# Kernel optimization log

Hardware: AMD Instinct MI355X
Metric: run time of the kernel (lower is better)

Reference implementation:

```python
import jax, jax.numpy as jnp
import numpy as np

TOP_K = 2          # routed top_k = top_k - num_shared_experts = 3 - 1
CAP_FACTOR = 1.1   # capacity_factor


def setup_inputs() -> dict:
    key = jax.random.key(0)
    ks = jax.random.split(key, 12)
    B, S, D, E = 4, 2048, 1024, 7
    s = 0.02
    return {
        "x": jax.random.normal(ks[0], (B, S, D), jnp.float32),
        "noise": jax.random.normal(ks[1], (B, S, E), jnp.float32),
        "Wr": jax.random.normal(ks[2], (D, E)) * s, "br": jnp.zeros((E,)),
        "Wn": jax.random.normal(ks[3], (D, E)) * s, "bn": jnp.zeros((E,)),
        "W1": jax.random.normal(ks[4], (E, D, D)) * s, "b1": jnp.zeros((E, D)),
        "W2": jax.random.normal(ks[5], (E, D, D)) * s, "b2": jnp.zeros((E, D)),
        "Ws1": jax.random.normal(ks[6], (D, D)) * s, "bs1": jnp.zeros((D,)),
        "Ws2": jax.random.normal(ks[7], (D, D)) * s, "bs2": jnp.zeros((D,)),
    }


def reference(x, noise, Wr, br, Wn, bn, W1, b1, W2, b2, Ws1, bs1, Ws2, bs2):
    B, S, D = x.shape
    E = Wr.shape[1]
    N = B * S
    C = int(N * TOP_K / E * CAP_FACTOR)  # per-expert capacity (static)

    # shared expert (Dropout inactive at inference)
    x_shared = jax.nn.relu(x @ Ws1 + bs1) @ Ws2 + bs2

    # --- noisy top-k router ---
    logits = x @ Wr + br
    noisy = logits + noise * jax.nn.softplus(x @ Wn + bn)
    vals, idx = jax.lax.top_k(noisy, TOP_K)                    # [B,S,K]
    onehot = jax.nn.one_hot(idx, E, dtype=x.dtype)             # [B,S,K,E]
    probs_k = jax.nn.softmax(vals, axis=-1)                    # softmax over -inf-masked logits == softmax over top-k vals
    router_probs = jnp.einsum('bske,bsk->bse', onehot, probs_k)
    expert_mask = onehot.sum(-2)
    lbl = E * (router_probs.mean((0, 1)) * expert_mask.mean((0, 1))).sum()

    # --- capacity-limited dispatch, first-come-first-served in flat token order ---
    flat_x = x.reshape(N, D)
    flat_g = router_probs.reshape(N, E)
    m = (expert_mask.reshape(N, E) > 0).T                      # [E,N] token->expert assignment
    pos = jnp.cumsum(m.astype(jnp.int32), axis=1) - 1          # slot within expert
    valid = m & (pos < C)
    token = jnp.arange(N, dtype=jnp.int32)
    dest = jnp.where(valid, jnp.arange(E, dtype=jnp.int32)[:, None] * C + pos, E * C)
    idxs = jnp.full((E * C + 1,), N, dtype=jnp.int32)
    idxs = idxs.at[dest.reshape(-1)].set(jnp.broadcast_to(token, (E, N)).reshape(-1))
    idxs = idxs[:E * C].reshape(E, C)                          # token id per slot, N = padding

    xpad = jnp.concatenate([flat_x, jnp.zeros((1, D), x.dtype)], axis=0)
    gpad = jnp.concatenate([flat_g, jnp.zeros((1, E), x.dtype)], axis=0)
    xe = xpad[idxs]                                            # [E,C,D]
    h = jax.nn.relu(jnp.einsum('ecd,edh->ech', xe, W1) + b1[:, None, :])
    out = jnp.einsum('ech,ehd->ecd', h, W2) + b2[:, None, :]
    g = (gpad[idxs] * jnp.eye(E, dtype=x.dtype)[:, None, :]).sum(-1)  # [E,C] gate per slot
    slot_valid = (idxs < N).astype(x.dtype)
    weighted = out * (g * slot_valid)[..., None]

    upd = jnp.zeros((N + 1, D), x.dtype).at[idxs.reshape(-1)].add(weighted.reshape(-1, D))[:N]
    final = upd.reshape(B, S, D) + x_shared
    return final, lbl
```

## Files before the change

kernel.cpp:

```cpp
#include <hip/hip_runtime.h>
#include <math.h>

typedef unsigned short u16;
typedef __attribute__((ext_vector_type(4))) float f32x4;
typedef __bf16 bf16x8 __attribute__((ext_vector_type(8)));

#define NTOK 8192
#define DDIM 1024
#define NEXP 7
#define CAPC 2574
#define CPAD 2688
#define EBLK 1176
#define TBLK 1688

__device__ inline float bf2f(u16 u) {
    union { unsigned int i; float f; } c; c.i = ((unsigned int)u) << 16; return c.f;
}
__device__ inline u16 f2bf(float f) {
    union { float f; unsigned int i; } c; c.f = f;
    unsigned int u = c.i;
    unsigned int r = (u + 0x7fffu + ((u >> 16) & 1u)) >> 16;
    return (u16)r;
}

__device__ inline void gl2lds16(const u16* g, const u16* l) {
    __builtin_amdgcn_global_load_lds(
        (const __attribute__((address_space(1))) unsigned int*)g,
        (__attribute__((address_space(3))) unsigned int*)l, 16, 0, 0);
}

__global__ void k_zero(float* out, long n) {
    long i = (long)blockIdx.x * 256 + threadIdx.x;
    long stride = (long)gridDim.x * 256;
    for (; i < n; i += stride) out[i] = 0.f;
}

__global__ void k_prep(const float* __restrict__ x, u16* __restrict__ xb,
                       int* __restrict__ slot_token, u16* __restrict__ zrow,
                       const float* __restrict__ srcE, const float* __restrict__ srcS,
                       u16* __restrict__ Wt, u16* __restrict__ Wst) {
    int bid = blockIdx.x, tid = threadIdx.x;
    if (bid < 4096) {
        int gid = bid * 256 + tid;
        int i = gid * 8;
        float4 a = *(const float4*)(x + i);
        float4 b = *(const float4*)(x + i + 4);
        ushort4 o0; o0.x = f2bf(a.x); o0.y = f2bf(a.y); o0.z = f2bf(a.z); o0.w = f2bf(a.w);
        ushort4 o1; o1.x = f2bf(b.x); o1.y = f2bf(b.y); o1.z = f2bf(b.z); o1.w = f2bf(b.w);
        *(ushort4*)(xb + i) = o0;
        *(ushort4*)(xb + i + 4) = o1;
        if (gid < DDIM) zrow[gid] = 0;
        if (gid < NEXP * CPAD) slot_token[gid] = NTOK;
    } else {
        int tb = bid - 4096;
        int z = tb >> 9; int rem = tb & 511;
        int y = rem >> 2; int xq = rem & 3;
        const float* src; u16* dst;
        if (z < 7) { src = srcE + (long)z * 1048576; dst = Wt + (long)z * 1048576; }
        else       { src = srcS;                     dst = Wst; }
        int n = xq * 256 + tid;
        int k0 = y * 8;
        u16 v[8];
#pragma unroll
        for (int j = 0; j < 8; ++j) v[j] = f2bf(src[(long)(k0 + j) * 1024 + n]);
        ushort4 a; a.x = v[0]; a.y = v[1]; a.z = v[2]; a.w = v[3];
        ushort4 b; b.x = v[4]; b.y = v[5]; b.z = v[6]; b.w = v[7];
        *(ushort4*)(dst + (long)n * 1024 + k0) = a;
        *(ushort4*)(dst + (long)n * 1024 + k0 + 4) = b;
    }
}

__global__ void k_transpose(const float* __restrict__ srcE, const float* __restrict__ srcS,
                            u16* __restrict__ Wt, u16* __restrict__ Wst) {
    int z = blockIdx.z;
    const float* src; u16* dst;
    if (z < 7) { src = srcE + (long)z * 1048576; dst = Wt + (long)z * 1048576; }
    else       { src = srcS;                     dst = Wst; }
    int n = blockIdx.x * 256 + threadIdx.x;
    int k0 = blockIdx.y * 8;
    u16 v[8];
#pragma unroll
    for (int j = 0; j < 8; ++j) v[j] = f2bf(src[(long)(k0 + j) * 1024 + n]);
    ushort4 a; a.x = v[0]; a.y = v[1]; a.z = v[2]; a.w = v[3];
    ushort4 b; b.x = v[4]; b.y = v[5]; b.z = v[6]; b.w = v[7];
    *(ushort4*)(dst + (long)n * 1024 + k0) = a;
    *(ushort4*)(dst + (long)n * 1024 + k0 + 4) = b;
}

__global__ __launch_bounds__(256) void k_router(
    const float* __restrict__ x, const float* __restrict__ noise,
    const float* __restrict__ Wr, const float* __restrict__ br,
    const float* __restrict__ Wn, const float* __restrict__ bn,
    int* __restrict__ idx0, int* __restrict__ idx1,
    float* __restrict__ p0, float* __restrict__ p1) {
    __shared__ float swr[7168];
    __shared__ float swn[7168];
    int tid = threadIdx.x;
    for (int i = tid; i < 7168; i += 256) { swr[i] = Wr[i]; swn[i] = Wn[i]; }
    __syncthreads();
    int lane = tid & 63, wv = tid >> 6;
    int t = blockIdx.x * 4 + wv;
    double ar[7] = {0,0,0,0,0,0,0}, an[7] = {0,0,0,0,0,0,0};
    for (int j = 0; j < 16; ++j) {
        int d = j * 64 + lane;
        double xd = (double)x[t * 1024 + d];
#pragma unroll
        for (int e = 0; e < 7; ++e) {
            ar[e] += xd * (double)swr[d * 7 + e];
            an[e] += xd * (double)swn[d * 7 + e];
        }
    }
#pragma unroll
    for (int e = 0; e < 7; ++e) {
        for (int o = 32; o > 0; o >>= 1) {
            ar[e] += __shfl_xor(ar[e], o);
            an[e] += __shfl_xor(an[e], o);
        }
    }
    if (lane == 0) {
        double best = -1e300, second = -1e300; int b0 = 0, b1 = 0;
#pragma unroll
        for (int e = 0; e < 7; ++e) {
            double lg = ar[e] + (double)br[e];
            double z  = an[e] + (double)bn[e];
            double sp = (z > 30.0) ? (z + log1p(exp(-z))) : log1p(exp(z));
            double v  = lg + (double)noise[t * 7 + e] * sp;
            if (v > best)        { second = best; b1 = b0; best = v; b0 = e; }
            else if (v > second) { second = v; b1 = e; }
        }
        double ex = exp(second - best);
        idx0[t] = b0; idx1[t] = b1;
        p0[t] = (float)(1.0 / (1.0 + ex));
        p1[t] = (float)(ex / (1.0 + ex));
    }
}

__global__ void k_count(const int* __restrict__ idx0, const int* __restrict__ idx1,
                        const float* __restrict__ p0, const float* __restrict__ p1,
                        int* __restrict__ cntA, double* __restrict__ sumA) {
    int lane = threadIdx.x & 63;
    int chunk = (blockIdx.x * 256 + threadIdx.x) >> 6;
    int t = chunk * 64 + lane;
    int i0 = idx0[t], i1 = idx1[t];
    double q0 = (double)p0[t], q1 = (double)p1[t];
#pragma unroll
    for (int e = 0; e < 7; ++e) {
        unsigned long long m = __ballot((i0 == e) || (i1 == e));
        double q = (i0 == e ? q0 : 0.0) + (i1 == e ? q1 : 0.0);
        for (int o = 32; o > 0; o >>= 1) q += __shfl_xor(q, o);
        if (lane == 0) { cntA[e * 128 + chunk] = __popcll(m); sumA[e * 128 + chunk] = q; }
    }
}

__global__ void k_scanbase(const int* __restrict__ cntA, const double* __restrict__ sumA,
                           int* __restrict__ baseA, int* __restrict__ cnt,
                           float* __restrict__ out) {
    __shared__ int s[128];
    __shared__ double rd[128];
    __shared__ int rawc[7];
    __shared__ double ps[7];
    int tid = threadIdx.x;
    for (int e = 0; e < 7; ++e) {
        int v = 0;
        if (tid < 128) { v = cntA[e * 128 + tid]; s[tid] = v; }
        if (tid < 128) rd[tid] = sumA[e * 128 + tid];
        __syncthreads();
        for (int o = 1; o < 128; o <<= 1) {
            int add = 0;
            if (tid < 128 && tid >= o) add = s[tid - o];
            __syncthreads();
            if (tid < 128) s[tid] += add;
            __syncthreads();
        }
        if (tid < 128) baseA[e * 128 + tid] = s[tid] - v;
        if (tid == 127) { rawc[e] = s[127]; cnt[e] = (s[127] < CAPC) ? s[127] : CAPC; }
        for (int o = 64; o > 0; o >>= 1) {
            if (tid < o) rd[tid] += rd[tid + o];
            __syncthreads();
        }
        if (tid == 0) ps[e] = rd[0];
        __syncthreads();
    }
    if (tid == 0) {
        double acc = 0.0;
        for (int e = 0; e < 7; ++e) acc += ps[e] * (double)rawc[e];
        out[(long)NTOK * DDIM] = (float)(7.0 * acc / (8192.0 * 8192.0));
    }
}

__global__ void k_assign(const int* __restrict__ idx0, const int* __restrict__ idx1,
                         const int* __restrict__ baseA, int* __restrict__ slot_token,
                         int* __restrict__ ts0, int* __restrict__ ts1) {
    int lane = threadIdx.x & 63;
    int chunk = (blockIdx.x * 256 + threadIdx.x) >> 6;
    int t = chunk * 64 + lane;
    int i0 = idx0[t], i1 = idx1[t];
    int myts0 = -1, myts1 = -1;
    unsigned long long lt = (1ull << lane) - 1ull;
#pragma unroll
    for (int e = 0; e < 7; ++e) {
        bool has = (i0 == e) || (i1 == e);
        unsigned long long m = __ballot(has);
        int pre = __popcll(m & lt);
        int pos = baseA[e * 128 + chunk] + pre;
        if (has && pos < CAPC) {
            int slot = e * CPAD + pos;
            slot_token[slot] = t;
            if (i0 == e) myts0 = slot; else myts1 = slot;
        }
    }
    ts0[t] = myts0; ts1[t] = myts1;
}

template <bool GATHER, bool MODE_H>
__global__ __launch_bounds__(256) void k_gemm(
    const u16* __restrict__ AbaseE, const u16* __restrict__ AbaseS,
    const int* __restrict__ gidx, const u16* __restrict__ zrow,
    const u16* __restrict__ WtE, const u16* __restrict__ WtS,
    const float* __restrict__ biasE, const float* __restrict__ biasS,
    u16* __restrict__ outE, u16* __restrict__ outS,
    const int* __restrict__ cnt) {
    __shared__ __align__(16) u16 ldsA[128 * 64];
    __shared__ __align__(16) u16 ldsB[128 * 64];
    int bid = blockIdx.x;
    int tid = threadIdx.x, lane = tid & 63, wv = tid >> 6;
    int lrow = lane >> 3, lkg = lane & 7;
    int kgs = lkg ^ lrow;

    int e = 0, my, nx;
    const u16* Ab; const u16* Bb; const float* bias; u16* outp;
    bool gather = false;
    if (bid < EBLK) {
        e = bid / 168; int r = bid % 168; my = r >> 3; nx = r & 7;
        if (my * 128 >= cnt[e]) return;
        Ab = AbaseE + (GATHER ? 0L : (long)e * CPAD * 1024);
        Bb = WtE + ((long)e << 20);
        bias = biasE + e * 1024;
        outp = outE + (long)e * CPAD * 1024;
        gather = GATHER;
    } else {
        int sb = bid - EBLK; my = sb >> 3; nx = sb & 7;
        Ab = AbaseS; Bb = WtS; bias = biasS; outp = outS;
    }
    int m0 = my * 128, n0 = nx * 128;

    const u16* arow[4];
    const u16* brow[4];
#pragma unroll
    for (int i = 0; i < 4; ++i) {
        int r = (wv * 4 + i) * 8 + lrow;
        if (gather) {
            int tok = gidx[e * CPAD + m0 + r];
            arow[i] = (tok < NTOK) ? (AbaseE + (long)tok * DDIM) : zrow;
        } else {
            arow[i] = Ab + (long)(m0 + r) * DDIM;
        }
        brow[i] = Bb + (long)(n0 + r) * DDIM;
    }
    f32x4 acc[4][4];
#pragma unroll
    for (int a = 0; a < 4; ++a)
#pragma unroll
        for (int b = 0; b < 4; ++b) { f32x4 z = {0.f, 0.f, 0.f, 0.f}; acc[a][b] = z; }

    int wm = (wv >> 1) * 64, wn = (wv & 1) * 64;
    int rl = lane & 15, quad = lane >> 4;

    for (int k0 = 0; k0 < 1024; k0 += 64) {
#pragma unroll
        for (int i = 0; i < 4; ++i) {
            gl2lds16(arow[i] + k0 + kgs * 8, &ldsA[(wv * 4 + i) * 512]);
            gl2lds16(brow[i] + k0 + kgs * 8, &ldsB[(wv * 4 + i) * 512]);
        }
        __syncthreads();
#pragma unroll
        for (int ks = 0; ks < 2; ++ks) {
            int kg = ks * 4 + quad;
            bf16x8 af[4], bf[4];
#pragma unroll
            for (int mi = 0; mi < 4; ++mi) {
                int row = wm + mi * 16 + rl;
                af[mi] = *(const bf16x8*)&ldsA[row * 64 + (kg ^ (row & 7)) * 8];
            }
#pragma unroll
            for (int ni = 0; ni < 4; ++ni) {
                int row = wn + ni * 16 + rl;
                bf[ni] = *(const bf16x8*)&ldsB[row * 64 + (kg ^ (row & 7)) * 8];
            }
#pragma unroll
            for (int mi = 0; mi < 4; ++mi)
#pragma unroll
                for (int ni = 0; ni < 4; ++ni)
                    acc[mi][ni] = __builtin_amdgcn_mfma_f32_16x16x32_bf16(
                        af[mi], bf[ni], acc[mi][ni], 0, 0, 0);
        }
        __syncthreads();
    }
#pragma unroll
    for (int ni = 0; ni < 4; ++ni) {
        int col = n0 + wn + ni * 16 + rl;
        float bv = bias[col];
#pragma unroll
        for (int mi = 0; mi < 4; ++mi) {
            int rowb = m0 + wm + mi * 16 + quad * 4;
#pragma unroll
            for (int r = 0; r < 4; ++r) {
                float v = acc[mi][ni][r] + bv;
                if constexpr (MODE_H) v = v > 0.f ? v : 0.f;
                outp[(long)(rowb + r) * DDIM + col] = f2bf(v);
            }
        }
    }
}

__global__ __launch_bounds__(256) void k_combine(
    const u16* __restrict__ Xs, const u16* __restrict__ OutE,
    const int* __restrict__ ts0, const int* __restrict__ ts1,
    const float* __restrict__ p0, const float* __restrict__ p1,
    float* __restrict__ out) {
    int b = blockIdx.x;
    int d = threadIdx.x * 4;
    long base = (long)b * DDIM + d;
    ushort4 xs4 = *(const ushort4*)(Xs + base);
    float r0 = bf2f(xs4.x), r1 = bf2f(xs4.y), r2 = bf2f(xs4.z), r3 = bf2f(xs4.w);
    int s0 = ts0[b], s1 = ts1[b];
    if (s0 >= 0) {
        float g = p0[b];
        ushort4 o4 = *(const ushort4*)(OutE + (long)s0 * DDIM + d);
        r0 += g * bf2f(o4.x); r1 += g * bf2f(o4.y); r2 += g * bf2f(o4.z); r3 += g * bf2f(o4.w);
    }
    if (s1 >= 0) {
        float g = p1[b];
        ushort4 o4 = *(const ushort4*)(OutE + (long)s1 * DDIM + d);
        r0 += g * bf2f(o4.x); r1 += g * bf2f(o4.y); r2 += g * bf2f(o4.z); r3 += g * bf2f(o4.w);
    }
    float4 w; w.x = r0; w.y = r1; w.z = r2; w.w = r3;
    *(float4*)(out + base) = w;
}

extern "C" void kernel_launch(void* const* d_in, const int* in_sizes, int n_in,
                              void* d_out, int out_size, void* d_ws, size_t ws_size,
                              hipStream_t stream) {
    const float* x    = (const float*)d_in[0];
    const float* noise= (const float*)d_in[1];
    const float* Wr   = (const float*)d_in[2];
    const float* br   = (const float*)d_in[3];
    const float* Wn   = (const float*)d_in[4];
    const float* bn   = (const float*)d_in[5];
    const float* W1   = (const float*)d_in[6];
    const float* b1   = (const float*)d_in[7];
    const float* W2   = (const float*)d_in[8];
    const float* b2   = (const float*)d_in[9];
    const float* Ws1  = (const float*)d_in[10];
    const float* bs1  = (const float*)d_in[11];
    const float* Ws2  = (const float*)d_in[12];
    const float* bs2  = (const float*)d_in[13];
    float* out = (float*)d_out;
    char* ws = (char*)d_ws;

    size_t off = 0;
    auto alloc = [&](size_t bytes) { size_t o = off; off += (bytes + 255) & ~(size_t)255; return o; };
    u16*  Wt   = (u16*)(ws + alloc(7ull * 1048576 * 2));
    u16*  Wst  = (u16*)(ws + alloc(1048576ull * 2));
    u16*  xb   = (u16*)(ws + alloc((size_t)NTOK * 1024 * 2));
    u16*  He   = (u16*)(ws + alloc((size_t)NEXP * CPAD * 1024 * 2));
    u16*  Hs   = (u16*)(ws + alloc((size_t)NTOK * 1024 * 2));
    u16*  OutE = (u16*)(ws + alloc((size_t)NEXP * CPAD * 1024 * 2));
    u16*  Xs   = (u16*)(ws + alloc((size_t)NTOK * 1024 * 2));
    int*  idx0 = (int*)(ws + alloc(NTOK * 4));
    int*  idx1 = (int*)(ws + alloc(NTOK * 4));
    float* p0  = (float*)(ws + alloc(NTOK * 4));
    float* p1  = (float*)(ws + alloc(NTOK * 4));
    int*  ts0  = (int*)(ws + alloc(NTOK * 4));
    int*  ts1  = (int*)(ws + alloc(NTOK * 4));
    int*  slot_token = (int*)(ws + alloc(NEXP * CPAD * 4));
    int*  cntA = (int*)(ws + alloc(7 * 128 * 4));
    int*  baseA= (int*)(ws + alloc(7 * 128 * 4));
    double* sumA = (double*)(ws + alloc(7 * 128 * 8));
    int*  cnt    = (int*)(ws + alloc(8 * 4));
    u16*  zrow   = (u16*)(ws + alloc(1024 * 2));

    if (off > ws_size) {
        k_zero<<<2048, 256, 0, stream>>>(out, (long)out_size);
        return;
    }

    k_prep<<<8192, 256, 0, stream>>>(x, xb, slot_token, zrow, W1, Ws1, Wt, Wst);
    k_router<<<2048, 256, 0, stream>>>(x, noise, Wr, br, Wn, bn, idx0, idx1, p0, p1);
    k_count<<<32, 256, 0, stream>>>(idx0, idx1, p0, p1, cntA, sumA);
    k_scanbase<<<1, 256, 0, stream>>>(cntA, sumA, baseA, cnt, out);
    k_assign<<<32, 256, 0, stream>>>(idx0, idx1, baseA, slot_token, ts0, ts1);

    k_gemm<true, true><<<TBLK, 256, 0, stream>>>(
        xb, xb, slot_token, zrow, Wt, Wst, b1, bs1, He, Hs, cnt);

    k_transpose<<<dim3(4, 128, 8), 256, 0, stream>>>(W2, Ws2, Wt, Wst);

    k_gemm<false, false><<<TBLK, 256, 0, stream>>>(
        He, Hs, nullptr, zrow, Wt, Wst, b2, bs2, OutE, Xs, cnt);

    k_combine<<<NTOK, 256, 0, stream>>>(Xs, OutE, ts0, ts1, p0, p1, out);
    (void)in_sizes; (void)n_in; (void)out_size;
}
```

Measured before the change: 424.5 us.

## Fold W2 transpose into prep kernel, split router into dot and tail kernels

When the workspace has room, the W2/Ws2 transpose-to-bf16 now runs inside the prep kernel into separate buffers instead of as a standalone launch between the two GEMMs. The router is split: a 512-thread dot-product kernel writes raw double logits, and a new tail kernel does softplus, top-2, softmax and the per-chunk counting, which replaces k_count. This cuts one launch from the critical path between the GEMMs and lets the transpose overlap with the x conversion. It costs extra workspace and a round trip of the logits through global memory.

New measurement: 402.2 us. 5.3% less time.

```diff
diff --git a/kernel.cpp b/kernel.cpp
--- a/kernel.cpp
+++ b/kernel.cpp
@@ -37,8 +37,10 @@
 
 __global__ void k_prep(const float* __restrict__ x, u16* __restrict__ xb,
                        int* __restrict__ slot_token, u16* __restrict__ zrow,
-                       const float* __restrict__ srcE, const float* __restrict__ srcS,
-                       u16* __restrict__ Wt, u16* __restrict__ Wst) {
+                       const float* __restrict__ W1, const float* __restrict__ Ws1,
+                       u16* __restrict__ Wt, u16* __restrict__ Wst,
+                       const float* __restrict__ W2, const float* __restrict__ Ws2,
+                       u16* __restrict__ Wt2, u16* __restrict__ Wst2) {
     int bid = blockIdx.x, tid = threadIdx.x;
     if (bid < 4096) {
         int gid = bid * 256 + tid;
@@ -51,23 +53,28 @@
         *(ushort4*)(xb + i + 4) = o1;
         if (gid < DDIM) zrow[gid] = 0;
         if (gid < NEXP * CPAD) slot_token[gid] = NTOK;
-    } else {
-        int tb = bid - 4096;
-        int z = tb >> 9; int rem = tb & 511;
-        int y = rem >> 2; int xq = rem & 3;
-        const float* src; u16* dst;
-        if (z < 7) { src = srcE + (long)z * 1048576; dst = Wt + (long)z * 1048576; }
-        else       { src = srcS;                     dst = Wst; }
-        int n = xq * 256 + tid;
-        int k0 = y * 8;
-        u16 v[8];
-#pragma unroll
-        for (int j = 0; j < 8; ++j) v[j] = f2bf(src[(long)(k0 + j) * 1024 + n]);
-        ushort4 a; a.x = v[0]; a.y = v[1]; a.z = v[2]; a.w = v[3];
-        ushort4 b; b.x = v[4]; b.y = v[5]; b.z = v[6]; b.w = v[7];
-        *(ushort4*)(dst + (long)n * 1024 + k0) = a;
-        *(ushort4*)(dst + (long)n * 1024 + k0 + 4) = b;
-    }
+        return;
+    }
+    int phase2 = (bid >= 8192);
+    int tb = bid - (phase2 ? 8192 : 4096);
+    const float* srcE = phase2 ? W2 : W1;
+    const float* srcS = phase2 ? Ws2 : Ws1;
+    u16* dE = phase2 ? Wt2 : Wt;
+    u16* dS = phase2 ? Wst2 : Wst;
+    int z = tb >> 9; int rem = tb & 511;
+    int y = rem >> 2; int xq = rem & 3;
+    const float* src; u16* dst;
+    if (z < 7) { src = srcE + (long)z * 1048576; dst = dE + (long)z * 1048576; }
+    else       { src = srcS;                     dst = dS; }
+    int n = xq * 256 + tid;
+    int k0 = y * 8;
+    u16 v[8];
+#pragma unroll
+    for (int j = 0; j < 8; ++j) v[j] = f2bf(src[(long)(k0 + j) * 1024 + n]);
+    ushort4 a; a.x = v[0]; a.y = v[1]; a.z = v[2]; a.w = v[3];
+    ushort4 b; b.x = v[4]; b.y = v[5]; b.z = v[6]; b.w = v[7];
+    *(ushort4*)(dst + (long)n * 1024 + k0) = a;
+    *(ushort4*)(dst + (long)n * 1024 + k0 + 4) = b;
 }
 
 __global__ void k_transpose(const float* __restrict__ srcE, const float* __restrict__ srcS,
@@ -87,19 +94,17 @@
     *(ushort4*)(dst + (long)n * 1024 + k0 + 4) = b;
 }
 
-__global__ __launch_bounds__(256) void k_router(
-    const float* __restrict__ x, const float* __restrict__ noise,
-    const float* __restrict__ Wr, const float* __restrict__ br,
-    const float* __restrict__ Wn, const float* __restrict__ bn,
-    int* __restrict__ idx0, int* __restrict__ idx1,
-    float* __restrict__ p0, float* __restrict__ p1) {
+__global__ __launch_bounds__(512) void k_router(
+    const float* __restrict__ x,
+    const float* __restrict__ Wr, const float* __restrict__ Wn,
+    double* __restrict__ arO, double* __restrict__ anO) {
     __shared__ float swr[7168];
     __shared__ float swn[7168];
     int tid = threadIdx.x;
-    for (int i = tid; i < 7168; i += 256) { swr[i] = Wr[i]; swn[i] = Wn[i]; }
+    for (int i = tid; i < 7168; i += 512) { swr[i] = Wr[i]; swn[i] = Wn[i]; }
     __syncthreads();
     int lane = tid & 63, wv = tid >> 6;
-    int t = blockIdx.x * 4 + wv;
+    int t = blockIdx.x * 8 + wv;
     double ar[7] = {0,0,0,0,0,0,0}, an[7] = {0,0,0,0,0,0,0};
     for (int j = 0; j < 16; ++j) {
         int d = j * 64 + lane;
@@ -118,35 +123,39 @@
         }
     }
     if (lane == 0) {
-        double best = -1e300, second = -1e300; int b0 = 0, b1 = 0;
-#pragma unroll
-        for (int e = 0; e < 7; ++e) {
-            double lg = ar[e] + (double)br[e];
-            double z  = an[e] + (double)bn[e];
-            double sp = (z > 30.0) ? (z + log1p(exp(-z))) : log1p(exp(z));
-            double v  = lg + (double)noise[t * 7 + e] * sp;
-            if (v > best)        { second = best; b1 = b0; best = v; b0 = e; }
-            else if (v > second) { second = v; b1 = e; }
-        }
-        double ex = exp(second - best);
-        idx0[t] = b0; idx1[t] = b1;
-        p0[t] = (float)(1.0 / (1.0 + ex));
-        p1[t] = (float)(ex / (1.0 + ex));
-    }
-}
-
-__global__ void k_count(const int* __restrict__ idx0, const int* __restrict__ idx1,
-                        const float* __restrict__ p0, const float* __restrict__ p1,
-                        int* __restrict__ cntA, double* __restrict__ sumA) {
+#pragma unroll
+        for (int e = 0; e < 7; ++e) { arO[t * 7 + e] = ar[e]; anO[t * 7 + e] = an[e]; }
+    }
+}
+
+__global__ void k_tail(const double* __restrict__ arO, const double* __restrict__ anO,
+                       const float* __restrict__ noise,
+                       const float* __restrict__ br, const float* __restrict__ bn,
+                       int* __restrict__ idx0, int* __restrict__ idx1,
+                       float* __restrict__ p0, float* __restrict__ p1,
+                       int* __restrict__ cntA, double* __restrict__ sumA) {
+    int t = blockIdx.x * 256 + threadIdx.x;
     int lane = threadIdx.x & 63;
-    int chunk = (blockIdx.x * 256 + threadIdx.x) >> 6;
-    int t = chunk * 64 + lane;
-    int i0 = idx0[t], i1 = idx1[t];
-    double q0 = (double)p0[t], q1 = (double)p1[t];
+    double best = -1e300, second = -1e300; int b0 = 0, b1 = 0;
 #pragma unroll
     for (int e = 0; e < 7; ++e) {
-        unsigned long long m = __ballot((i0 == e) || (i1 == e));
-        double q = (i0 == e ? q0 : 0.0) + (i1 == e ? q1 : 0.0);
+        double lg = arO[t * 7 + e] + (double)br[e];
+        double z  = anO[t * 7 + e] + (double)bn[e];
+        double sp = (z > 30.0) ? (z + log1p(exp(-z))) : log1p(exp(z));
+        double v  = lg + (double)noise[t * 7 + e] * sp;
+        if (v > best)        { second = best; b1 = b0; best = v; b0 = e; }
+        else if (v > second) { second = v; b1 = e; }
+    }
+    double ex = exp(second - best);
+    float q0 = (float)(1.0 / (1.0 + ex));
+    float q1 = (float)(ex / (1.0 + ex));
+    idx0[t] = b0; idx1[t] = b1; p0[t] = q0; p1[t] = q1;
+    int chunk = t >> 6;
+    double dq0 = (double)q0, dq1 = (double)q1;
+#pragma unroll
+    for (int e = 0; e < 7; ++e) {
+        unsigned long long m = __ballot((b0 == e) || (b1 == e));
+        double q = (b0 == e ? dq0 : 0.0) + (b1 == e ? dq1 : 0.0);
         for (int o = 32; o > 0; o >>= 1) q += __shfl_xor(q, o);
         if (lane == 0) { cntA[e * 128 + chunk] = __popcll(m); sumA[e * 128 + chunk] = q; }
     }
@@ -379,25 +388,34 @@
     double* sumA = (double*)(ws + alloc(7 * 128 * 8));
     int*  cnt    = (int*)(ws + alloc(8 * 4));
     u16*  zrow   = (u16*)(ws + alloc(1024 * 2));
-
-    if (off > ws_size) {
+    double* arO  = (double*)(ws + alloc((size_t)NTOK * 7 * 8));
+    double* anO  = (double*)(ws + alloc((size_t)NTOK * 7 * 8));
+    size_t base_off = off;
+    u16*  Wt2  = (u16*)(ws + alloc(7ull * 1048576 * 2));
+    u16*  Wst2 = (u16*)(ws + alloc(1048576ull * 2));
+
+    if (base_off > ws_size) {
         k_zero<<<2048, 256, 0, stream>>>(out, (long)out_size);
         return;
     }
-
-    k_prep<<<8192, 256, 0, stream>>>(x, xb, slot_token, zrow, W1, Ws1, Wt, Wst);
-    k_router<<<2048, 256, 0, stream>>>(x, noise, Wr, br, Wn, bn, idx0, idx1, p0, p1);
-    k_count<<<32, 256, 0, stream>>>(idx0, idx1, p0, p1, cntA, sumA);
+    bool sep = (off <= ws_size);
+    if (!sep) { Wt2 = Wt; Wst2 = Wst; }
+
+    k_prep<<<sep ? 12288 : 8192, 256, 0, stream>>>(
+        x, xb, slot_token, zrow, W1, Ws1, Wt, Wst, W2, Ws2, Wt2, Wst2);
+    k_router<<<1024, 512, 0, stream>>>(x, Wr, Wn, arO, anO);
+    k_tail<<<32, 256, 0, stream>>>(arO, anO, noise, br, bn, idx0, idx1, p0, p1, cntA, sumA);
     k_scanbase<<<1, 256, 0, stream>>>(cntA, sumA, baseA, cnt, out);
     k_assign<<<32, 256, 0, stream>>>(idx0, idx1, baseA, slot_token, ts0, ts1);
 
     k_gemm<true, true><<<TBLK, 256, 0, stream>>>(
         xb, xb, slot_token, zrow, Wt, Wst, b1, bs1, He, Hs, cnt);
 
-    k_transpose<<<dim3(4, 128, 8), 256, 0, stream>>>(W2, Ws2, Wt, Wst);
+    if (!sep)
+        k_transpose<<<dim3(4, 128, 8), 256, 0, stream>>>(W2, Ws2, Wt, Wst);
 
     k_gemm<false, false><<<TBLK, 256, 0, stream>>>(
-        He, Hs, nullptr, zrow, Wt, Wst, b2, bs2, OutE, Xs, cnt);
+        He, Hs, nullptr, zrow, Wt2, Wst2, b2, bs2, OutE, Xs, cnt);
 
     k_combine<<<NTOK, 256, 0, stream>>>(Xs, OutE, ts0, ts1, p0, p1, out);
     (void)in_sizes; (void)n_in; (void)out_size;
```
